# Optimization experiments

Hardware: AMD Instinct MI355X
Metric: run time of the kernel (lower is better)

The kernel has to match this reference:

```python
import jax, jax.numpy as jnp
import numpy as np

L, D, H, V, T_BLK, B, T = 6, 768, 12, 32000, 1024, 4, 1024
HD = D // H          # head size = 64
FF = 4 * D           # FFN hidden
EPS = 1e-5


def _ln(x, g, b):
    m = x.mean(-1, keepdims=True)
    v = ((x - m) ** 2).mean(-1, keepdims=True)
    return (x - m) * jax.lax.rsqrt(v + EPS) * g + b


def _attn(q_in, kv_in, wqkv, wo, bo, causal):
    # wqkv: [3, D, D]; heads batched (equivalent to concat of per-head Linear outputs)
    Bq, Tq, _ = q_in.shape
    Tk = kv_in.shape[1]
    q = (q_in @ wqkv[0]).reshape(Bq, Tq, H, HD)
    k = (kv_in @ wqkv[1]).reshape(Bq, Tk, H, HD)
    v = (kv_in @ wqkv[2]).reshape(Bq, Tk, H, HD)
    wei = jnp.einsum('bqhd,bkhd->bhqk', q, k) * (HD ** -0.5)
    if causal:
        mask = jnp.tril(jnp.ones((Tq, Tk), dtype=bool))
        wei = jnp.where(mask, wei, -jnp.inf)
    wei = jax.nn.softmax(wei, axis=-1)
    out = jnp.einsum('bhqk,bkhd->bqhd', wei, v).reshape(Bq, Tq, D)
    return out @ wo + bo


def _ffn(x, w1, b1, w2, b2):
    return jax.nn.relu(x @ w1 + b1) @ w2 + b2


def _forward(idx, encoder_input,
             enc_tok, enc_pos, enc_qkv, enc_wo, enc_bo, enc_w1, enc_b1, enc_w2, enc_b2,
             enc_ln1g, enc_ln1b, enc_ln2g, enc_ln2b, enc_lnfg, enc_lnfb,
             dec_tok, dec_pos, dec_qkv, dec_wo, dec_bo, dec_cqkv, dec_cwo, dec_cbo,
             dec_w1, dec_b1, dec_w2, dec_b2,
             dec_ln1g, dec_ln1b, dec_ln2g, dec_ln2b, dec_ln3g, dec_ln3b,
             dec_lnfg, dec_lnfb, lm_w, lm_b):
    # ---- encoder (NOTE: original Head always applies causal tril, so encoder is causal) ----
    Te = encoder_input.shape[1]
    x = enc_tok[encoder_input] + enc_pos[:Te]
    for i in range(L):
        h = _ln(x, enc_ln1g[i], enc_ln1b[i])
        x = x + _attn(h, h, enc_qkv[i], enc_wo[i], enc_bo[i], causal=True)
        h = _ln(x, enc_ln2g[i], enc_ln2b[i])
        x = x + _ffn(h, enc_w1[i], enc_b1[i], enc_w2[i], enc_b2[i])
    enc_out = _ln(x, enc_lnfg, enc_lnfb)
    # ---- decoder ----
    Td = idx.shape[1]
    y = dec_tok[idx] + dec_pos[:Td]
    for i in range(L):
        h = _ln(y, dec_ln1g[i], dec_ln1b[i])
        y = y + _attn(h, h, dec_qkv[i], dec_wo[i], dec_bo[i], causal=True)
        h = _ln(y, dec_ln2g[i], dec_ln2b[i])
        y = y + _attn(h, enc_out, dec_cqkv[i], dec_cwo[i], dec_cbo[i], causal=False)
        h = _ln(y, dec_ln3g[i], dec_ln3b[i])
        y = y + _ffn(h, dec_w1[i], dec_b1[i], dec_w2[i], dec_b2[i])
    y = _ln(y, dec_lnfg, dec_lnfb)
    return y @ lm_w + lm_b  # logits [B, T, V]


def setup_inputs() -> dict:
    key = jax.random.key(0)
    keys = iter(jax.random.split(key, 80))
    def nrm(shape, s=0.02):
        return jax.random.normal(next(keys), shape, dtype=jnp.float32) * s
    z = lambda shape: jnp.zeros(shape, jnp.float32)
    o = lambda shape: jnp.ones(shape, jnp.float32)
    inp = {}
    inp['idx'] = jax.random.randint(next(keys), (B, T), 0, V)
    inp['encoder_input'] = jax.random.randint(next(keys), (B, T), 0, V)
    # encoder params
    inp['enc_tok'] = nrm((V, D)); inp['enc_pos'] = nrm((T_BLK, D))
    inp['enc_qkv'] = nrm((L, 3, D, D)); inp['enc_wo'] = nrm((L, D, D)); inp['enc_bo'] = z((L, D))
    inp['enc_w1'] = nrm((L, D, FF)); inp['enc_b1'] = z((L, FF))
    inp['enc_w2'] = nrm((L, FF, D)); inp['enc_b2'] = z((L, D))
    inp['enc_ln1g'] = o((L, D)); inp['enc_ln1b'] = z((L, D))
    inp['enc_ln2g'] = o((L, D)); inp['enc_ln2b'] = z((L, D))
    inp['enc_lnfg'] = o((D,)); inp['enc_lnfb'] = z((D,))
    # decoder params
    inp['dec_tok'] = nrm((V, D)); inp['dec_pos'] = nrm((T_BLK, D))
    inp['dec_qkv'] = nrm((L, 3, D, D)); inp['dec_wo'] = nrm((L, D, D)); inp['dec_bo'] = z((L, D))
    inp['dec_cqkv'] = nrm((L, 3, D, D)); inp['dec_cwo'] = nrm((L, D, D)); inp['dec_cbo'] = z((L, D))
    inp['dec_w1'] = nrm((L, D, FF)); inp['dec_b1'] = z((L, FF))
    inp['dec_w2'] = nrm((L, FF, D)); inp['dec_b2'] = z((L, D))
    inp['dec_ln1g'] = o((L, D)); inp['dec_ln1b'] = z((L, D))
    inp['dec_ln2g'] = o((L, D)); inp['dec_ln2b'] = z((L, D))
    inp['dec_ln3g'] = o((L, D)); inp['dec_ln3b'] = z((L, D))
    inp['dec_lnfg'] = o((D,)); inp['dec_lnfb'] = z((D,))
    inp['lm_w'] = nrm((D, V)); inp['lm_b'] = z((V,))
    return inp


def reference(idx, encoder_input,
              enc_tok, enc_pos, enc_qkv, enc_wo, enc_bo, enc_w1, enc_b1, enc_w2, enc_b2,
              enc_ln1g, enc_ln1b, enc_ln2g, enc_ln2b, enc_lnfg, enc_lnfb,
              dec_tok, dec_pos, dec_qkv, dec_wo, dec_bo, dec_cqkv, dec_cwo, dec_cbo,
              dec_w1, dec_b1, dec_w2, dec_b2,
              dec_ln1g, dec_ln1b, dec_ln2g, dec_ln2b, dec_ln3g, dec_ln3b,
              dec_lnfg, dec_lnfb, lm_w, lm_b):
    return _forward(idx, encoder_input,
                    enc_tok, enc_pos, enc_qkv, enc_wo, enc_bo, enc_w1, enc_b1, enc_w2, enc_b2,
                    enc_ln1g, enc_ln1b, enc_ln2g, enc_ln2b, enc_lnfg, enc_lnfb,
                    dec_tok, dec_pos, dec_qkv, dec_wo, dec_bo, dec_cqkv, dec_cwo, dec_cbo,
                    dec_w1, dec_b1, dec_w2, dec_b2,
                    dec_ln1g, dec_ln1b, dec_ln2g, dec_ln2b, dec_ln3g, dec_ln3b,
                    dec_lnfg, dec_lnfb, lm_w, lm_b)
```

## Files before the change

### kernel.cpp

```cpp
#include <hip/hip_runtime.h>


typedef __bf16 bf16x8 __attribute__((ext_vector_type(8)));
typedef float  f32x4  __attribute__((ext_vector_type(4)));
typedef unsigned short u16x4 __attribute__((ext_vector_type(4)));
typedef unsigned short u16x8 __attribute__((ext_vector_type(8)));

constexpr int Lc = 6, Dc = 768, Hc = 12, HDc = 64, Vc = 32000;
constexpr int Bc = 4, Tc = 1024, FFc = 3072;
constexpr int Mtot = Bc * Tc;

static __device__ __forceinline__ unsigned short f2bf(float f) {
  union { float f; unsigned u; } x; x.f = f;
  unsigned r = x.u + 0x7fffu + ((x.u >> 16) & 1u);
  return (unsigned short)(r >> 16);
}
static __device__ __forceinline__ float bf2f(unsigned short s) {
  union { unsigned u; float f; } c; c.u = (unsigned)s << 16; return c.f;
}

static __device__ __forceinline__ void gl_lds16(const unsigned short* g, unsigned short* l) {
  __builtin_amdgcn_global_load_lds(
      (const __attribute__((address_space(1))) unsigned int*)g,
      (__attribute__((address_space(3))) unsigned int*)l, 16, 0, 0);
}

template <int N> static __device__ __forceinline__ void wait_vm() {
  if constexpr (N == 0)      asm volatile("s_waitcnt vmcnt(0)" ::: "memory");
  else if constexpr (N == 2) asm volatile("s_waitcnt vmcnt(2)" ::: "memory");
  else if constexpr (N == 3) asm volatile("s_waitcnt vmcnt(3)" ::: "memory");
  else if constexpr (N == 4) asm volatile("s_waitcnt vmcnt(4)" ::: "memory");
}

static __device__ __forceinline__ float blockReduceSum(float v, float* red) {
  #pragma unroll
  for (int o = 32; o; o >>= 1) v += __shfl_xor(v, o, 64);
  int w = threadIdx.x >> 6;
  __syncthreads();
  if ((threadIdx.x & 63) == 0) red[w] = v;
  __syncthreads();
  return red[0] + red[1] + red[2] + red[3];
}

__global__ __launch_bounds__(256) void wconv_k(const float* __restrict__ W,
                                               unsigned short* __restrict__ WT,
                                               int K, int N) {
  __shared__ float t[32][33];
  const long zoff = (long)blockIdx.z * K * N;
  const int k0 = blockIdx.x * 32, n0 = blockIdx.y * 32;
  const int tid = threadIdx.x;
  const int rr = tid >> 3;
  const int cc = (tid & 7) * 4;
  f32x4 v = *reinterpret_cast<const f32x4*>(W + zoff + (long)(k0 + rr) * N + n0 + cc);
  #pragma unroll
  for (int j = 0; j < 4; j++) t[rr][cc + j] = v[j];
  __syncthreads();
  u16x4 o;
  #pragma unroll
  for (int j = 0; j < 4; j++) o[j] = f2bf(t[cc + j][rr]);
  *reinterpret_cast<u16x4*>(WT + zoff + (long)(n0 + rr) * K + k0 + cc) = o;
}

__global__ __launch_bounds__(256) void vtrans_k(const unsigned short* __restrict__ V,
                                                unsigned short* __restrict__ VT) {
  __shared__ unsigned short t[64][65];
  const int bh = blockIdx.y;
  const int b = bh / Hc, h = bh % Hc;
  const int t0 = blockIdx.x * 64;
  const int tid = threadIdx.x;
  const int rr = tid >> 3;
  const int c8 = (tid & 7) * 8;
  #pragma unroll
  for (int rep = 0; rep < 2; rep++) {
    int row = rep * 32 + rr;
    u16x8 v = *reinterpret_cast<const u16x8*>(V + (long)(b * Tc + t0 + row) * Dc + h * HDc + c8);
    #pragma unroll
    for (int j = 0; j < 8; j++) t[row][c8 + j] = v[j];
  }
  __syncthreads();
  #pragma unroll
  for (int rep = 0; rep < 2; rep++) {
    int hd = rep * 32 + rr;
    u16x8 o;
    #pragma unroll
    for (int j = 0; j < 8; j++) o[j] = t[c8 + j][hd];
    *reinterpret_cast<u16x8*>(VT + ((long)bh * HDc + hd) * Tc + t0 + c8) = o;
  }
}

__global__ __launch_bounds__(256) void embed_k(const int* __restrict__ idx,
                                               const float* __restrict__ tok,
                                               const float* __restrict__ pos,
                                               float* __restrict__ out) {
  const long row = blockIdx.x;
  const int t = (int)(row % Tc);
  const long id = idx[row];
  #pragma unroll
  for (int j = 0; j < 3; j++) {
    int e = threadIdx.x + j * 256;
    out[row * Dc + e] = tok[id * Dc + e] + pos[(long)t * Dc + e];
  }
}

__global__ __launch_bounds__(256) void ln_k(const float* __restrict__ X,
                                            const float* __restrict__ g,
                                            const float* __restrict__ bta,
                                            unsigned short* __restrict__ out) {
  __shared__ float red[4];
  const long row = blockIdx.x;
  const int tid = threadIdx.x;
  float v[3];
  #pragma unroll
  for (int j = 0; j < 3; j++) v[j] = X[row * Dc + tid + j * 256];
  float s = v[0] + v[1] + v[2];
  s = blockReduceSum(s, red);
  float mean = s * (1.f / 768.f);
  float q = 0.f;
  #pragma unroll
  for (int j = 0; j < 3; j++) { float d = v[j] - mean; q += d * d; }
  q = blockReduceSum(q, red);
  float rstd = rsqrtf(q * (1.f / 768.f) + 1e-5f);
  #pragma unroll
  for (int j = 0; j < 3; j++) {
    int e = tid + j * 256;
    out[row * Dc + e] = f2bf((v[j] - mean) * rstd * g[e] + bta[e]);
  }
}

template <bool CAUSAL>
__global__ __launch_bounds__(256) void flash_k(
    const unsigned short* __restrict__ Q,
    const unsigned short* __restrict__ K,
    const unsigned short* __restrict__ VT,
    unsigned short* __restrict__ O) {
  __shared__ __align__(16) unsigned short Ks[128 * 64];
  __shared__ __align__(16) unsigned short Vs[64 * 128];
  __shared__ __align__(16) unsigned short Ps[4][32 * 128];

  const int tid = threadIdx.x;
  const int lane = tid & 63;
  const int w = tid >> 6;
  const int lane16 = lane & 15;
  const int l4 = lane >> 4;
  const int bh = blockIdx.y;
  const int b = bh / Hc, h = bh % Hc;
  const int q0 = blockIdx.x * 128;

  const unsigned short* Qb = Q + ((long)b * Tc) * Dc + h * HDc;
  const unsigned short* Kb = K + ((long)b * Tc) * Dc + h * HDc;
  const unsigned short* Vb = VT + (long)bh * HDc * Tc;
  unsigned short* Ob = O + ((long)b * Tc) * Dc + h * HDc;

  bf16x8 qf[2][2];
  #pragma unroll
  for (int m = 0; m < 2; m++)
    #pragma unroll
    for (int kk = 0; kk < 2; kk++) {
      u16x8 raw = *reinterpret_cast<const u16x8*>(
          Qb + (long)(q0 + w * 32 + m * 16 + lane16) * Dc + kk * 32 + l4 * 8);
      bf16x8 f;
      #pragma unroll
      for (int j = 0; j < 8; j++) f[j] = (__bf16)(bf2f(raw[j]) * 0.125f);
      qf[m][kk] = f;
    }

  float mrow[2][4], lrow[2][4];
  f32x4 accO[2][4];
  #pragma unroll
  for (int m = 0; m < 2; m++)
    #pragma unroll
    for (int r = 0; r < 4; r++) { mrow[m][r] = -1e30f; lrow[m][r] = 0.f; }
  #pragma unroll
  for (int m = 0; m < 2; m++)
    #pragma unroll
    for (int d4 = 0; d4 < 4; d4++)
      #pragma unroll
      for (int r = 0; r < 4; r++) accO[m][d4][r] = 0.f;

  const int nch = CAUSAL ? (blockIdx.x + 1) : (Tc / 128);
  for (int c = 0; c < nch; c++) {
    const int k0 = c * 128;
    __syncthreads();
    #pragma unroll
    for (int it = 0; it < 4; it++) {
      int u = (it * 4 + w) * 64 + lane;
      int r = u >> 3, s = u & 7;
      gl_lds16(Kb + (long)(k0 + r) * Dc + ((s ^ (r & 7)) * 8), &Ks[(it * 4 + w) * 512]);
      int r2 = u >> 4, s2 = u & 15;
      gl_lds16(Vb + (long)r2 * Tc + k0 + ((s2 ^ (r2 & 7)) * 8), &Vs[(it * 4 + w) * 512]);
    }
    __syncthreads();

    f32x4 sacc[2][8];
    #pragma unroll
    for (int m = 0; m < 2; m++)
      #pragma unroll
      for (int n = 0; n < 8; n++)
        #pragma unroll
        for (int r = 0; r < 4; r++) sacc[m][n][r] = 0.f;
    #pragma unroll
    for (int n = 0; n < 8; n++) {
      int row = n * 16 + lane16;
      #pragma unroll
      for (int kk = 0; kk < 2; kk++) {
        bf16x8 kf = *reinterpret_cast<const bf16x8*>(
            &Ks[row * 64 + (((kk * 4 + l4) ^ (row & 7)) * 8)]);
        sacc[0][n] = __builtin_amdgcn_mfma_f32_16x16x32_bf16(qf[0][kk], kf, sacc[0][n], 0, 0, 0);
        sacc[1][n] = __builtin_amdgcn_mfma_f32_16x16x32_bf16(qf[1][kk], kf, sacc[1][n], 0, 0, 0);
      }
    }

    if (CAUSAL && c == nch - 1) {
      #pragma unroll
      for (int m = 0; m < 2; m++)
        #pragma unroll
        for (int n = 0; n < 8; n++)
          #pragma unroll
          for (int r = 0; r < 4; r++) {
            int kcol = k0 + n * 16 + lane16;
            int q = q0 + w * 32 + m * 16 + l4 * 4 + r;
            if (kcol > q) sacc[m][n][r] = -1e30f;
          }
    }

    #pragma unroll
    for (int m = 0; m < 2; m++)
      #pragma unroll
      for (int r = 0; r < 4; r++) {
        float smax = sacc[m][0][r];
        #pragma unroll
        for (int n = 1; n < 8; n++) smax = fmaxf(smax, sacc[m][n][r]);
        #pragma unroll
        for (int off = 1; off < 16; off <<= 1) smax = fmaxf(smax, __shfl_xor(smax, off, 64));
        float mold = mrow[m][r];
        float mnew = fmaxf(mold, smax);
        float sc = __expf(mold - mnew);
        float psum = 0.f;
        unsigned short pv[8];
        #pragma unroll
        for (int n = 0; n < 8; n++) {
          float p = __expf(sacc[m][n][r] - mnew);
          psum += p;
          pv[n] = f2bf(p);
        }
        #pragma unroll
        for (int off = 1; off < 16; off <<= 1) psum += __shfl_xor(psum, off, 64);
        lrow[m][r] = lrow[m][r] * sc + psum;
        mrow[m][r] = mnew;
        #pragma unroll
        for (int d4 = 0; d4 < 4; d4++) accO[m][d4][r] *= sc;
        int prow = m * 16 + l4 * 4 + r;
        #pragma unroll
        for (int n = 0; n < 8; n++) {
          int col = n * 16 + lane16;
          Ps[w][prow * 128 + (((col >> 3) ^ (prow & 7)) * 8) + (col & 7)] = pv[n];
        }
      }

    #pragma unroll
    for (int kk = 0; kk < 4; kk++) {
      bf16x8 pa[2];
      #pragma unroll
      for (int m = 0; m < 2; m++) {
        int arow = m * 16 + lane16;
        pa[m] = *reinterpret_cast<const bf16x8*>(
            &Ps[w][arow * 128 + (((kk * 4 + l4) ^ (arow & 7)) * 8)]);
      }
      #pragma unroll
      for (int d4 = 0; d4 < 4; d4++) {
        int vrow = d4 * 16 + lane16;
        bf16x8 vf = *reinterpret_cast<const bf16x8*>(
            &Vs[vrow * 128 + (((kk * 4 + l4) ^ (vrow & 7)) * 8)]);
        accO[0][d4] = __builtin_amdgcn_mfma_f32_16x16x32_bf16(pa[0], vf, accO[0][d4], 0, 0, 0);
        accO[1][d4] = __builtin_amdgcn_mfma_f32_16x16x32_bf16(pa[1], vf, accO[1][d4], 0, 0, 0);
      }
    }
  }

  #pragma unroll
  for (int m = 0; m < 2; m++)
    #pragma unroll
    for (int r = 0; r < 4; r++) {
      float inv = 1.f / lrow[m][r];
      int q = q0 + w * 32 + m * 16 + l4 * 4 + r;
      #pragma unroll
      for (int d4 = 0; d4 < 4; d4++)
        Ob[(long)q * Dc + d4 * 16 + lane16] = f2bf(accO[m][d4][r] * inv);
    }
}

template <int BM, int BN, int MF, int NF, int MINW, int CHUNKG,
          bool HASBIAS, bool RELU, bool HASRES, bool OUTBF>
__global__ __launch_bounds__(256, MINW) void gemm_k(
    const unsigned short* __restrict__ A, long sAb, long sAh, int lda,
    const unsigned short* __restrict__ BT, long sBb, long sBh, int ldb,
    void* Cp, long sCb, long sCh, int ldc,
    const float* __restrict__ bias,
    const float* __restrict__ Res, int ldr,
    const unsigned short* __restrict__ A2,
    int K, int nH, float alpha) {
  constexpr int AI = BM / 64;
  constexpr int BI = BN / 64;
  constexpr int VC = AI + BI;
  __shared__ __align__(16) unsigned short As[2][BM * 32];
  __shared__ __align__(16) unsigned short Bs[2][BN * 32];

  const int tid = threadIdx.x;
  const int lane = tid & 63;
  const int w = tid >> 6;
  const int wr = w >> 1, wc = w & 1;
  const int lane16 = lane & 15;
  const int l4 = lane >> 4;

  const int z = blockIdx.z;
  const int bb = z / nH, hh = z % nH;
  const unsigned short* Abase = (A2 != nullptr && hh != 0) ? A2 : A;
  const long offA = sAb * bb + sAh * hh;
  const long offB = sBb * bb + sBh * hh;
  const long offC = sCb * bb + sCh * hh;

  const int gx = gridDim.x;
  const int gy = gridDim.y;
  const int nwg = gx * gy;
  const int id = blockIdx.y * gx + blockIdx.x;
  const int q8 = nwg >> 3, r8 = nwg & 7;
  const int xcd = id & 7, ord = id >> 3;
  const int swz = (xcd < r8 ? xcd * (q8 + 1) : r8 * (q8 + 1) + (xcd - r8) * q8) + ord;
  int m0, n0;
  if constexpr (CHUNKG > 0) {
    const int span = gy * CHUNKG;
    const int xg = swz / span;
    const int rem = swz - xg * span;
    const int yy = rem / CHUNKG;
    const int xi = rem - yy * CHUNKG;
    m0 = (xg * CHUNKG + xi) * BM;
    n0 = yy * BN;
  } else {
    m0 = (swz % gx) * BM;
    n0 = (swz / gx) * BN;
  }

  const int srow = lane >> 2;
  const int sslot = ((lane & 3) ^ ((srow >> 1) & 3)) * 8;

  const unsigned short* aP[AI];
  #pragma unroll
  for (int j = 0; j < AI; j++)
    aP[j] = Abase + offA + (long)(m0 + w * (BM / 4) + j * 16 + srow) * lda + sslot;
  const unsigned short* bP[BI];
  #pragma unroll
  for (int j = 0; j < BI; j++)
    bP[j] = BT + offB + (long)(n0 + w * (BN / 4) + j * 16 + srow) * ldb + sslot;

  f32x4 acc[MF][NF];
  #pragma unroll
  for (int m = 0; m < MF; m++)
    #pragma unroll
    for (int n = 0; n < NF; n++)
      #pragma unroll
      for (int r = 0; r < 4; r++) acc[m][n][r] = 0.f;

  auto STAGE = [&](int buf, int k0) {
    #pragma unroll
    for (int j = 0; j < AI; j++)
      gl_lds16(aP[j] + k0, &As[buf][(w * (BM / 4) + j * 16) * 32]);
    #pragma unroll
    for (int j = 0; j < BI; j++)
      gl_lds16(bP[j] + k0, &Bs[buf][(w * (BN / 4) + j * 16) * 32]);
  };

  const int nt = K / 32;
  STAGE(0, 0);
  int cur = 0;
  for (int t = 0; t < nt; t++) {
    if (t + 1 < nt) { STAGE(cur ^ 1, (t + 1) * 32); wait_vm<VC>(); }
    else            { wait_vm<0>(); }
    __builtin_amdgcn_sched_barrier(0);
    __builtin_amdgcn_s_barrier();
    __builtin_amdgcn_sched_barrier(0);

    bf16x8 afr[MF], bfr[NF];
    #pragma unroll
    for (int n = 0; n < NF; n++) {
      int row = wc * NF * 16 + n * 16 + lane16;
      bfr[n] = *reinterpret_cast<const bf16x8*>(
          &Bs[cur][row * 32 + ((l4 ^ ((row >> 1) & 3)) * 8)]);
    }
    #pragma unroll
    for (int m = 0; m < MF; m++) {
      int row = wr * MF * 16 + m * 16 + lane16;
      afr[m] = *reinterpret_cast<const bf16x8*>(
          &As[cur][row * 32 + ((l4 ^ ((row >> 1) & 3)) * 8)]);
    }
    __builtin_amdgcn_s_setprio(1);
    #pragma unroll
    for (int m = 0; m < MF; m++)
      #pragma unroll
      for (int n = 0; n < NF; n++)
        acc[m][n] = __builtin_amdgcn_mfma_f32_16x16x32_bf16(afr[m], bfr[n], acc[m][n], 0, 0, 0);
    __builtin_amdgcn_s_setprio(0);

    asm volatile("s_waitcnt lgkmcnt(0)" ::: "memory");
    __builtin_amdgcn_sched_barrier(0);
    __builtin_amdgcn_s_barrier();
    cur ^= 1;
  }

  const int r0 = m0 + wr * MF * 16;
  const int c0 = n0 + wc * NF * 16;
  #pragma unroll
  for (int m = 0; m < MF; m++) {
    #pragma unroll
    for (int n = 0; n < NF; n++) {
      #pragma unroll
      for (int r = 0; r < 4; r++) {
        int rr = r0 + m * 16 + l4 * 4 + r;
        int cc = c0 + n * 16 + lane16;
        float v = acc[m][n][r] * alpha;
        if constexpr (HASBIAS) v += bias[cc];
        if constexpr (RELU) v = fmaxf(v, 0.f);
        if constexpr (HASRES) v += Res[offC + (long)rr * ldr + cc];
        if constexpr (OUTBF) ((unsigned short*)Cp)[offC + (long)rr * ldc + cc] = f2bf(v);
        else                 ((float*)Cp)[offC + (long)rr * ldc + cc] = v;
      }
    }
  }
}

extern "C" void kernel_launch(void* const* d_in, const int* in_sizes, int n_in,
                              void* d_out, int out_size, void* d_ws, size_t ws_size,
                              hipStream_t stream) {
  (void)in_sizes; (void)n_in; (void)out_size;

  const int*   idx      = (const int*)d_in[0];
  const int*   enc_in   = (const int*)d_in[1];
  const float* enc_tok  = (const float*)d_in[2];
  const float* enc_pos  = (const float*)d_in[3];
  const float* enc_qkv  = (const float*)d_in[4];
  const float* enc_wo   = (const float*)d_in[5];
  const float* enc_bo   = (const float*)d_in[6];
  const float* enc_w1   = (const float*)d_in[7];
  const float* enc_b1   = (const float*)d_in[8];
  const float* enc_w2   = (const float*)d_in[9];
  const float* enc_b2   = (const float*)d_in[10];
  const float* enc_ln1g = (const float*)d_in[11];
  const float* enc_ln1b = (const float*)d_in[12];
  const float* enc_ln2g = (const float*)d_in[13];
  const float* enc_ln2b = (const float*)d_in[14];
  const float* enc_lnfg = (const float*)d_in[15];
  const float* enc_lnfb = (const float*)d_in[16];
  const float* dec_tok  = (const float*)d_in[17];
  const float* dec_pos  = (const float*)d_in[18];
  const float* dec_qkv  = (const float*)d_in[19];
  const float* dec_wo   = (const float*)d_in[20];
  const float* dec_bo   = (const float*)d_in[21];
  const float* dec_cqkv = (const float*)d_in[22];
  const float* dec_cwo  = (const float*)d_in[23];
  const float* dec_cbo  = (const float*)d_in[24];
  const float* dec_w1   = (const float*)d_in[25];
  const float* dec_b1   = (const float*)d_in[26];
  const float* dec_w2   = (const float*)d_in[27];
  const float* dec_b2   = (const float*)d_in[28];
  const float* dec_ln1g = (const float*)d_in[29];
  const float* dec_ln1b = (const float*)d_in[30];
  const float* dec_ln2g = (const float*)d_in[31];
  const float* dec_ln2b = (const float*)d_in[32];
  const float* dec_ln3g = (const float*)d_in[33];
  const float* dec_ln3b = (const float*)d_in[34];
  const float* dec_lnfg = (const float*)d_in[35];
  const float* dec_lnfb = (const float*)d_in[36];
  const float* lm_w     = (const float*)d_in[37];
  const float* lm_b     = (const float*)d_in[38];

  constexpr long De2 = (long)Dc * Dc;
  constexpr long DF  = (long)Dc * FFc;

  unsigned short* wcache = (unsigned short*)d_out;
  size_t woff = 0;
  auto take = [&](size_t n) { unsigned short* p = wcache + woff; woff += n; return p; };
  unsigned short* enc_qkvT  = take(18ul * De2);
  unsigned short* enc_woT   = take(6ul * De2);
  unsigned short* enc_w1T   = take(6ul * DF);
  unsigned short* enc_w2T   = take(6ul * DF);
  unsigned short* dec_qkvT  = take(18ul * De2);
  unsigned short* dec_woT   = take(6ul * De2);
  unsigned short* dec_cqkvT = take(18ul * De2);
  unsigned short* dec_cwoT  = take(6ul * De2);
  unsigned short* dec_w1T   = take(6ul * DF);
  unsigned short* dec_w2T   = take(6ul * DF);

  char* ws = (char*)d_ws;
  const size_t need = (size_t)Dc * Vc * 2 + 2ull * Mtot * Dc * 4 + 3ull * Mtot * Dc * 2 +
                      3ull * Mtot * Dc * 2 + (size_t)Mtot * FFc * 2 + (size_t)Mtot * Dc * 2 +
                      (size_t)Bc * Hc * HDc * Tc * 2 + 4096;
  if (ws_size < need) return;
  auto takeW = [&](size_t bytes) { char* p = ws; ws += (bytes + 255) & ~255ull; return p; };
  unsigned short* lm_wT = (unsigned short*)takeW((size_t)Dc * Vc * 2);
  float* xe             = (float*)takeW((size_t)Mtot * Dc * 4);
  float* xd             = (float*)takeW((size_t)Mtot * Dc * 4);
  unsigned short* hbf   = (unsigned short*)takeW((size_t)Mtot * Dc * 2);
  unsigned short* qkvb  = (unsigned short*)takeW(3ull * Mtot * Dc * 2);
  unsigned short* ao    = (unsigned short*)takeW((size_t)Mtot * Dc * 2);
  unsigned short* mid   = (unsigned short*)takeW((size_t)Mtot * FFc * 2);
  unsigned short* eo    = (unsigned short*)takeW((size_t)Mtot * Dc * 2);
  unsigned short* vT    = (unsigned short*)takeW((size_t)Bc * Hc * HDc * Tc * 2);
  unsigned short* qb = qkvb;
  unsigned short* kb = qkvb + (size_t)Mtot * Dc;
  unsigned short* vb = qkvb + 2ull * Mtot * Dc;

  const dim3 TB(256);

  wconv_k<<<dim3(Dc/32, Dc/32, 18), TB, 0, stream>>>(enc_qkv, enc_qkvT, Dc, Dc);
  wconv_k<<<dim3(Dc/32, Dc/32,  6), TB, 0, stream>>>(enc_wo,  enc_woT,  Dc, Dc);
  wconv_k<<<dim3(Dc/32, FFc/32, 6), TB, 0, stream>>>(enc_w1,  enc_w1T,  Dc, FFc);
  wconv_k<<<dim3(FFc/32, Dc/32, 6), TB, 0, stream>>>(enc_w2,  enc_w2T,  FFc, Dc);
  wconv_k<<<dim3(Dc/32, Dc/32, 18), TB, 0, stream>>>(dec_qkv, dec_qkvT, Dc, Dc);
  wconv_k<<<dim3(Dc/32, Dc/32,  6), TB, 0, stream>>>(dec_wo,  dec_woT,  Dc, Dc);
  wconv_k<<<dim3(Dc/32, Dc/32, 18), TB, 0, stream>>>(dec_cqkv,dec_cqkvT,Dc, Dc);
  wconv_k<<<dim3(Dc/32, Dc/32,  6), TB, 0, stream>>>(dec_cwo, dec_cwoT, Dc, Dc);
  wconv_k<<<dim3(Dc/32, FFc/32, 6), TB, 0, stream>>>(dec_w1,  dec_w1T,  Dc, FFc);
  wconv_k<<<dim3(FFc/32, Dc/32, 6), TB, 0, stream>>>(dec_w2,  dec_w2T,  FFc, Dc);
  wconv_k<<<dim3(Dc/32, Vc/32,  1), TB, 0, stream>>>(lm_w,    lm_wT,    Dc, Vc);

  auto LN = [&](const float* X, const float* g, const float* b, unsigned short* o) {
    ln_k<<<dim3(Mtot), TB, 0, stream>>>(X, g, b, o);
  };
  auto QKV3 = [&](const unsigned short* Abf, const unsigned short* W3T) {
    gemm_k<128,64,4,2,4,0,false,false,false,true>
      <<<dim3(Mtot/128, Dc/64, 3), TB, 0, stream>>>(
        Abf, 0, 0, Dc, W3T, De2, 0, Dc,
        qkvb, (long)Mtot*Dc, 0, Dc, nullptr, nullptr, 0, nullptr, Dc, 1, 1.f);
  };
  auto CQKV = [&](const unsigned short* Abf, const unsigned short* WcT) {
    gemm_k<64,64,2,2,4,0,false,false,false,true>
      <<<dim3(Mtot/64, Dc/64, 3), TB, 0, stream>>>(
        Abf, 0, 0, Dc, WcT, 0, De2, Dc,
        qkvb, 0, (long)Mtot*Dc, Dc, nullptr, nullptr, 0, eo, Dc, 3, 1.f);
  };
  auto VT = [&]() {
    vtrans_k<<<dim3(Tc/64, Bc*Hc), TB, 0, stream>>>(vb, vT);
  };
  auto FLASH = [&](bool causal) {
    if (causal) flash_k<true ><<<dim3(Tc/128, Bc*Hc), TB, 0, stream>>>(qb, kb, vT, ao);
    else        flash_k<false><<<dim3(Tc/128, Bc*Hc), TB, 0, stream>>>(qb, kb, vT, ao);
  };
  auto ORES = [&](const unsigned short* Abf, const unsigned short* WT, const float* bias, float* X) {
    gemm_k<64,64,2,2,4,0,true,false,true,false>
      <<<dim3(Mtot/64, Dc/64, 1), TB, 0, stream>>>(
        Abf, 0, 0, Dc, WT, 0, 0, Dc,
        X, 0, 0, Dc, bias, X, Dc, nullptr, Dc, 1, 1.f);
  };
  auto FFN1 = [&](const unsigned short* Abf, const unsigned short* WT, const float* bias) {
    gemm_k<128,128,4,4,3,0,true,true,false,true>
      <<<dim3(Mtot/128, FFc/128, 1), TB, 0, stream>>>(
        Abf, 0, 0, Dc, WT, 0, 0, Dc,
        mid, 0, 0, FFc, bias, nullptr, 0, nullptr, Dc, 1, 1.f);
  };
  auto FFN2 = [&](const unsigned short* WT, const float* bias, float* X) {
    gemm_k<64,64,2,2,4,0,true,false,true,false>
      <<<dim3(Mtot/64, Dc/64, 1), TB, 0, stream>>>(
        mid, 0, 0, FFc, WT, 0, 0, FFc,
        X, 0, 0, Dc, bias, X, Dc, nullptr, FFc, 1, 1.f);
  };

  embed_k<<<dim3(Mtot), TB, 0, stream>>>(enc_in, enc_tok, enc_pos, xe);
  for (int i = 0; i < Lc; i++) {
    LN(xe, enc_ln1g + i * Dc, enc_ln1b + i * Dc, hbf);
    QKV3(hbf, enc_qkvT + (size_t)i * 3 * De2);
    VT(); FLASH(true);
    ORES(ao, enc_woT + (size_t)i * De2, enc_bo + i * Dc, xe);
    LN(xe, enc_ln2g + i * Dc, enc_ln2b + i * Dc, hbf);
    FFN1(hbf, enc_w1T + (size_t)i * DF, enc_b1 + i * FFc);
    FFN2(enc_w2T + (size_t)i * DF, enc_b2 + i * Dc, xe);
  }
  LN(xe, enc_lnfg, enc_lnfb, eo);

  embed_k<<<dim3(Mtot), TB, 0, stream>>>(idx, dec_tok, dec_pos, xd);
  for (int i = 0; i < Lc; i++) {
    LN(xd, dec_ln1g + i * Dc, dec_ln1b + i * Dc, hbf);
    QKV3(hbf, dec_qkvT + (size_t)i * 3 * De2);
    VT(); FLASH(true);
    ORES(ao, dec_woT + (size_t)i * De2, dec_bo + i * Dc, xd);
    LN(xd, dec_ln2g + i * Dc, dec_ln2b + i * Dc, hbf);
    CQKV(hbf, dec_cqkvT + (size_t)i * 3 * De2);
    VT(); FLASH(false);
    ORES(ao, dec_cwoT + (size_t)i * De2, dec_cbo + i * Dc, xd);
    LN(xd, dec_ln3g + i * Dc, dec_ln3b + i * Dc, hbf);
    FFN1(hbf, dec_w1T + (size_t)i * DF, dec_b1 + i * FFc);
    FFN2(dec_w2T + (size_t)i * DF, dec_b2 + i * Dc, xd);
  }
  LN(xd, dec_lnfg, dec_lnfb, hbf);

  gemm_k<128,128,4,4,4,16,true,false,false,false>
    <<<dim3(Mtot/128, Vc/128, 1), TB, 0, stream>>>(
      hbf, 0, 0, Dc, lm_wT, 0, 0, Dc,
      d_out, 0, 0, Vc, lm_b, nullptr, 0, nullptr, Dc, 1, 1.f);
}
```

Baseline: 3.939 ms.

## Add BK=64 K-tiling to GEMMs, retile FFN1, and batch weight conversion into one launch

The GEMM kernel now takes a K-tile depth template parameter. With BK=64 it stages two 32-wide K slices per barrier, using a new 8-way LDS XOR swizzle. This halves the number of barrier/wait iterations and doubles the async loads in flight per stage, at the cost of twice the LDS per buffer. FFN1 moves from 128x128 to 128x64 tiles with BK=64, and QKV3 drops its min-waves bound from 4 to 3. The eleven weight transpose/convert launches are merged into a single table-driven kernel to cut launch overhead.

Measured after the change: 3.848 ms. 2.3% less time.

```diff
diff --git a/kernel.cpp b/kernel.cpp
--- a/kernel.cpp
+++ b/kernel.cpp
@@ -30,6 +30,7 @@
   else if constexpr (N == 2) asm volatile("s_waitcnt vmcnt(2)" ::: "memory");
   else if constexpr (N == 3) asm volatile("s_waitcnt vmcnt(3)" ::: "memory");
   else if constexpr (N == 4) asm volatile("s_waitcnt vmcnt(4)" ::: "memory");
+  else if constexpr (N == 6) asm volatile("s_waitcnt vmcnt(6)" ::: "memory");
 }
 
 static __device__ __forceinline__ float blockReduceSum(float v, float* red) {
@@ -42,23 +43,40 @@
   return red[0] + red[1] + red[2] + red[3];
 }
 
-__global__ __launch_bounds__(256) void wconv_k(const float* __restrict__ W,
-                                               unsigned short* __restrict__ WT,
-                                               int K, int N) {
+struct WcTab {
+  const float* src[11];
+  unsigned short* dst[11];
+  int Kt[11], Nt[11];
+  int start[12];
+};
+
+__global__ __launch_bounds__(256) void wconv_all_k(WcTab tab) {
   __shared__ float t[32][33];
-  const long zoff = (long)blockIdx.z * K * N;
-  const int k0 = blockIdx.x * 32, n0 = blockIdx.y * 32;
+  const int tb = blockIdx.x;
+  int e = 0;
+  #pragma unroll
+  for (int i = 1; i < 11; i++) if (tb >= tab.start[i]) e = i;
+  const int local = tb - tab.start[e];
+  const int Kt = tab.Kt[e], Nt = tab.Nt[e];
+  const int per = Kt * Nt;
+  const int z = local / per;
+  const int rem = local - z * per;
+  const int k0 = (rem / Nt) * 32, n0 = (rem % Nt) * 32;
+  const int K = Kt * 32, N = Nt * 32;
+  const float* W = tab.src[e] + (long)z * K * N;
+  unsigned short* WT = tab.dst[e] + (long)z * K * N;
+
   const int tid = threadIdx.x;
   const int rr = tid >> 3;
   const int cc = (tid & 7) * 4;
-  f32x4 v = *reinterpret_cast<const f32x4*>(W + zoff + (long)(k0 + rr) * N + n0 + cc);
+  f32x4 v = *reinterpret_cast<const f32x4*>(W + (long)(k0 + rr) * N + n0 + cc);
   #pragma unroll
   for (int j = 0; j < 4; j++) t[rr][cc + j] = v[j];
   __syncthreads();
   u16x4 o;
   #pragma unroll
   for (int j = 0; j < 4; j++) o[j] = f2bf(t[cc + j][rr]);
-  *reinterpret_cast<u16x4*>(WT + zoff + (long)(n0 + rr) * K + k0 + cc) = o;
+  *reinterpret_cast<u16x4*>(WT + (long)(n0 + rr) * K + k0 + cc) = o;
 }
 
 __global__ __launch_bounds__(256) void vtrans_k(const unsigned short* __restrict__ V,
@@ -289,7 +307,7 @@
     }
 }
 
-template <int BM, int BN, int MF, int NF, int MINW, int CHUNKG,
+template <int BM, int BN, int BK, int MF, int NF, int MINW, int CHUNKG,
           bool HASBIAS, bool RELU, bool HASRES, bool OUTBF>
 __global__ __launch_bounds__(256, MINW) void gemm_k(
     const unsigned short* __restrict__ A, long sAb, long sAh, int lda,
@@ -299,11 +317,12 @@
     const float* __restrict__ Res, int ldr,
     const unsigned short* __restrict__ A2,
     int K, int nH, float alpha) {
-  constexpr int AI = BM / 64;
-  constexpr int BI = BN / 64;
+  constexpr int RPI = 1024 / (2 * BK);
+  constexpr int AI = (BM / 4) / RPI;
+  constexpr int BI = (BN / 4) / RPI;
   constexpr int VC = AI + BI;
-  __shared__ __align__(16) unsigned short As[2][BM * 32];
-  __shared__ __align__(16) unsigned short Bs[2][BN * 32];
+  __shared__ __align__(16) unsigned short As[2][BM * BK];
+  __shared__ __align__(16) unsigned short Bs[2][BN * BK];
 
   const int tid = threadIdx.x;
   const int lane = tid & 63;
@@ -340,17 +359,23 @@
     n0 = (swz / gx) * BN;
   }
 
-  const int srow = lane >> 2;
-  const int sslot = ((lane & 3) ^ ((srow >> 1) & 3)) * 8;
+  int srow, sslot;
+  if constexpr (BK == 32) {
+    srow = lane >> 2;
+    sslot = ((lane & 3) ^ ((srow >> 1) & 3)) * 8;
+  } else {
+    srow = lane >> 3;
+    sslot = ((lane & 7) ^ (srow & 7)) * 8;
+  }
 
   const unsigned short* aP[AI];
   #pragma unroll
   for (int j = 0; j < AI; j++)
-    aP[j] = Abase + offA + (long)(m0 + w * (BM / 4) + j * 16 + srow) * lda + sslot;
+    aP[j] = Abase + offA + (long)(m0 + w * (BM / 4) + j * RPI + srow) * lda + sslot;
   const unsigned short* bP[BI];
   #pragma unroll
   for (int j = 0; j < BI; j++)
-    bP[j] = BT + offB + (long)(n0 + w * (BN / 4) + j * 16 + srow) * ldb + sslot;
+    bP[j] = BT + offB + (long)(n0 + w * (BN / 4) + j * RPI + srow) * ldb + sslot;
 
   f32x4 acc[MF][NF];
   #pragma unroll
@@ -363,42 +388,50 @@
   auto STAGE = [&](int buf, int k0) {
     #pragma unroll
     for (int j = 0; j < AI; j++)
-      gl_lds16(aP[j] + k0, &As[buf][(w * (BM / 4) + j * 16) * 32]);
+      gl_lds16(aP[j] + k0, &As[buf][(w * (BM / 4) + j * RPI) * BK]);
     #pragma unroll
     for (int j = 0; j < BI; j++)
-      gl_lds16(bP[j] + k0, &Bs[buf][(w * (BN / 4) + j * 16) * 32]);
-  };
-
-  const int nt = K / 32;
+      gl_lds16(bP[j] + k0, &Bs[buf][(w * (BN / 4) + j * RPI) * BK]);
+  };
+
+  auto kkey = [&](int row) -> int {
+    if constexpr (BK == 32) return (row >> 1) & 3;
+    else                    return row & 7;
+  };
+
+  const int nt = K / BK;
   STAGE(0, 0);
   int cur = 0;
   for (int t = 0; t < nt; t++) {
-    if (t + 1 < nt) { STAGE(cur ^ 1, (t + 1) * 32); wait_vm<VC>(); }
+    if (t + 1 < nt) { STAGE(cur ^ 1, (t + 1) * BK); wait_vm<VC>(); }
     else            { wait_vm<0>(); }
     __builtin_amdgcn_sched_barrier(0);
     __builtin_amdgcn_s_barrier();
     __builtin_amdgcn_sched_barrier(0);
 
-    bf16x8 afr[MF], bfr[NF];
-    #pragma unroll
-    for (int n = 0; n < NF; n++) {
-      int row = wc * NF * 16 + n * 16 + lane16;
-      bfr[n] = *reinterpret_cast<const bf16x8*>(
-          &Bs[cur][row * 32 + ((l4 ^ ((row >> 1) & 3)) * 8)]);
-    }
-    #pragma unroll
-    for (int m = 0; m < MF; m++) {
-      int row = wr * MF * 16 + m * 16 + lane16;
-      afr[m] = *reinterpret_cast<const bf16x8*>(
-          &As[cur][row * 32 + ((l4 ^ ((row >> 1) & 3)) * 8)]);
-    }
-    __builtin_amdgcn_s_setprio(1);
-    #pragma unroll
-    for (int m = 0; m < MF; m++)
-      #pragma unroll
-      for (int n = 0; n < NF; n++)
-        acc[m][n] = __builtin_amdgcn_mfma_f32_16x16x32_bf16(afr[m], bfr[n], acc[m][n], 0, 0, 0);
-    __builtin_amdgcn_s_setprio(0);
+    #pragma unroll
+    for (int kk = 0; kk < BK / 32; kk++) {
+      bf16x8 afr[MF], bfr[NF];
+      #pragma unroll
+      for (int n = 0; n < NF; n++) {
+        int row = wc * NF * 16 + n * 16 + lane16;
+        bfr[n] = *reinterpret_cast<const bf16x8*>(
+            &Bs[cur][row * BK + (((kk * 4 + l4) ^ kkey(row)) * 8)]);
+      }
+      #pragma unroll
+      for (int m = 0; m < MF; m++) {
+        int row = wr * MF * 16 + m * 16 + lane16;
+        afr[m] = *reinterpret_cast<const bf16x8*>(
+            &As[cur][row * BK + (((kk * 4 + l4) ^ kkey(row)) * 8)]);
+      }
+      __builtin_amdgcn_s_setprio(1);
+      #pragma unroll
+      for (int m = 0; m < MF; m++)
+        #pragma unroll
+        for (int n = 0; n < NF; n++)
+          acc[m][n] = __builtin_amdgcn_mfma_f32_16x16x32_bf16(afr[m], bfr[n], acc[m][n], 0, 0, 0);
+      __builtin_amdgcn_s_setprio(0);
+    }
 
     asm volatile("s_waitcnt lgkmcnt(0)" ::: "memory");
     __builtin_amdgcn_sched_barrier(0);
@@ -510,29 +543,36 @@
 
   const dim3 TB(256);
 
-  wconv_k<<<dim3(Dc/32, Dc/32, 18), TB, 0, stream>>>(enc_qkv, enc_qkvT, Dc, Dc);
-  wconv_k<<<dim3(Dc/32, Dc/32,  6), TB, 0, stream>>>(enc_wo,  enc_woT,  Dc, Dc);
-  wconv_k<<<dim3(Dc/32, FFc/32, 6), TB, 0, stream>>>(enc_w1,  enc_w1T,  Dc, FFc);
-  wconv_k<<<dim3(FFc/32, Dc/32, 6), TB, 0, stream>>>(enc_w2,  enc_w2T,  FFc, Dc);
-  wconv_k<<<dim3(Dc/32, Dc/32, 18), TB, 0, stream>>>(dec_qkv, dec_qkvT, Dc, Dc);
-  wconv_k<<<dim3(Dc/32, Dc/32,  6), TB, 0, stream>>>(dec_wo,  dec_woT,  Dc, Dc);
-  wconv_k<<<dim3(Dc/32, Dc/32, 18), TB, 0, stream>>>(dec_cqkv,dec_cqkvT,Dc, Dc);
-  wconv_k<<<dim3(Dc/32, Dc/32,  6), TB, 0, stream>>>(dec_cwo, dec_cwoT, Dc, Dc);
-  wconv_k<<<dim3(Dc/32, FFc/32, 6), TB, 0, stream>>>(dec_w1,  dec_w1T,  Dc, FFc);
-  wconv_k<<<dim3(FFc/32, Dc/32, 6), TB, 0, stream>>>(dec_w2,  dec_w2T,  FFc, Dc);
-  wconv_k<<<dim3(Dc/32, Vc/32,  1), TB, 0, stream>>>(lm_w,    lm_wT,    Dc, Vc);
+  WcTab tab;
+  tab.start[0] = 0;
+  auto ent = [&](int i, const float* s, unsigned short* d, int K, int N, int nz) {
+    tab.src[i] = s; tab.dst[i] = d; tab.Kt[i] = K / 32; tab.Nt[i] = N / 32;
+    tab.start[i + 1] = tab.start[i] + (K / 32) * (N / 32) * nz;
+  };
+  ent(0,  enc_qkv,  enc_qkvT,  Dc,  Dc, 18);
+  ent(1,  enc_wo,   enc_woT,   Dc,  Dc,  6);
+  ent(2,  enc_w1,   enc_w1T,   Dc,  FFc, 6);
+  ent(3,  enc_w2,   enc_w2T,   FFc, Dc,  6);
+  ent(4,  dec_qkv,  dec_qkvT,  Dc,  Dc, 18);
+  ent(5,  dec_wo,   dec_woT,   Dc,  Dc,  6);
+  ent(6,  dec_cqkv, dec_cqkvT, Dc,  Dc, 18);
+  ent(7,  dec_cwo,  dec_cwoT,  Dc,  Dc,  6);
+  ent(8,  dec_w1,   dec_w1T,   Dc,  FFc, 6);
+  ent(9,  dec_w2,   dec_w2T,   FFc, Dc,  6);
+  ent(10, lm_w,     lm_wT,     Dc,  Vc,  1);
+  wconv_all_k<<<dim3(tab.start[11]), TB, 0, stream>>>(tab);
 
   auto LN = [&](const float* X, const float* g, const float* b, unsigned short* o) {
     ln_k<<<dim3(Mtot), TB, 0, stream>>>(X, g, b, o);
   };
   auto QKV3 = [&](const unsigned short* Abf, const unsigned short* W3T) {
-    gemm_k<128,64,4,2,4,0,false,false,false,true>
+    gemm_k<128,64,64,4,2,3,0,false,false,false,true>
       <<<dim3(Mtot/128, Dc/64, 3), TB, 0, stream>>>(
         Abf, 0, 0, Dc, W3T, De2, 0, Dc,
         qkvb, (long)Mtot*Dc, 0, Dc, nullptr, nullptr, 0, nullptr, Dc, 1, 1.f);
   };
   auto CQKV = [&](const unsigned short* Abf, const unsigned short* WcT) {
-    gemm_k<64,64,2,2,4,0,false,false,false,true>
+    gemm_k<64,64,64,2,2,4,0,false,false,false,true>
       <<<dim3(Mtot/64, Dc/64, 3), TB, 0, stream>>>(
         Abf, 0, 0, Dc, WcT, 0, De2, Dc,
         qkvb, 0, (long)Mtot*Dc, Dc, nullptr, nullptr, 0, eo, Dc, 3, 1.f);
@@ -545,19 +585,19 @@
     else        flash_k<false><<<dim3(Tc/128, Bc*Hc), TB, 0, stream>>>(qb, kb, vT, ao);
   };
   auto ORES = [&](const unsigned short* Abf, const unsigned short* WT, const float* bias, float* X) {
-    gemm_k<64,64,2,2,4,0,true,false,true,false>
+    gemm_k<64,64,64,2,2,4,0,true,false,true,false>
       <<<dim3(Mtot/64, Dc/64, 1), TB, 0, stream>>>(
         Abf, 0, 0, Dc, WT, 0, 0, Dc,
         X, 0, 0, Dc, bias, X, Dc, nullptr, Dc, 1, 1.f);
   };
   auto FFN1 = [&](const unsigned short* Abf, const unsigned short* WT, const float* bias) {
-    gemm_k<128,128,4,4,3,0,true,true,false,true>
-      <<<dim3(Mtot/128, FFc/128, 1), TB, 0, stream>>>(
+    gemm_k<128,64,64,4,2,3,0,true,true,false,true>
+      <<<dim3(Mtot/128, FFc/64, 1), TB, 0, stream>>>(
         Abf, 0, 0, Dc, WT, 0, 0, Dc,
         mid, 0, 0, FFc, bias, nullptr, 0, nullptr, Dc, 1, 1.f);
   };
   auto FFN2 = [&](const unsigned short* WT, const float* bias, float* X) {
-    gemm_k<64,64,2,2,4,0,true,false,true,false>
+    gemm_k<64,64,64,2,2,4,0,true,false,true,false>
       <<<dim3(Mtot/64, Dc/64, 1), TB, 0, stream>>>(
         mid, 0, 0, FFc, WT, 0, 0, FFc,
         X, 0, 0, Dc, bias, X, Dc, nullptr, FFc, 1, 1.f);
@@ -591,7 +631,7 @@
   }
   LN(xd, dec_lnfg, dec_lnfb, hbf);
 
-  gemm_k<128,128,4,4,4,16,true,false,false,false>
+  gemm_k<128,128,32,4,4,4,16,true,false,false,false>
     <<<dim3(Mtot/128, Vc/128, 1), TB, 0, stream>>>(
       hbf, 0, 0, Dc, lm_wT, 0, 0, Dc,
       d_out, 0, 0, Vc, lm_b, nullptr, 0, nullptr, Dc, 1, 1.f);
```
